# Kernel optimization log

Measured on AMD Instinct MI355X. Metric: run time of the kernel, lower is better.

Reference implementation:

```python
import jax, jax.numpy as jnp
import numpy as np

N_HEAD = 16

def setup_inputs() -> dict:
    key = jax.random.key(0)
    kx, kq, kk, kv, kp = jax.random.split(key, 5)
    B, T, C = 4, 2048, 1024
    scale = 1.0 / np.sqrt(C)
    x = jax.random.normal(kx, (B, T, C), dtype=jnp.float32)
    Wq = jax.random.normal(kq, (C, C), dtype=jnp.float32) * scale
    Wk = jax.random.normal(kk, (C, C), dtype=jnp.float32) * scale
    Wv = jax.random.normal(kv, (C, C), dtype=jnp.float32) * scale
    Wp = jax.random.normal(kp, (C, C), dtype=jnp.float32) * scale
    return {"x": x, "Wq": Wq, "Wk": Wk, "Wv": Wv, "Wp": Wp}

def reference(x, Wq, Wk, Wv, Wp):
    B, T, C = x.shape
    H = N_HEAD
    D = C // H
    # projections (nn.Linear, no bias): x @ W^T
    q = (x @ Wq.T).reshape(B, T, H, D).transpose(0, 2, 1, 3)  # [B,H,T,D]
    k = (x @ Wk.T).reshape(B, T, H, D).transpose(0, 2, 1, 3)
    v = (x @ Wv.T).reshape(B, T, H, D).transpose(0, 2, 1, 3)
    att = jnp.einsum('bhqd,bhkd->bhqk', q, k) / jnp.sqrt(jnp.float32(D))
    causal = jnp.tril(jnp.ones((T, T), dtype=bool))
    att = jnp.where(causal, att, -jnp.inf)
    att = jax.nn.softmax(att, axis=-1)
    # dropout p=0.0 -> identity
    y = jnp.einsum('bhqk,bhkd->bhqd', att, v)  # [B,H,T,D]
    y = y.transpose(0, 2, 1, 3).reshape(B, T, C)
    return y @ Wp.T
```

## Files before the change

### kernel.cpp

```cpp
#include <hip/hip_runtime.h>

typedef __bf16 bfrag __attribute__((ext_vector_type(8)));
typedef __bf16 bh4 __attribute__((ext_vector_type(4)));
typedef float f4 __attribute__((ext_vector_type(4)));

#define AS1C(p) (const __attribute__((address_space(1))) void*)(p)
#define AS3(p)  (__attribute__((address_space(3))) void*)(p)

#define QSCALE 0.18033688011112042f

__device__ __forceinline__ void g2l16(const __bf16* g, __bf16* l) {
  __builtin_amdgcn_global_load_lds(AS1C(g), AS3(l), 16, 0, 0);
}

__global__ __launch_bounds__(256) void cvt5(
    const float* __restrict__ s0, const float* __restrict__ s1,
    const float* __restrict__ s2, const float* __restrict__ s3,
    const float* __restrict__ s4,
    __bf16* __restrict__ d0, __bf16* __restrict__ d1, __bf16* __restrict__ d2,
    __bf16* __restrict__ d3, __bf16* __restrict__ d4, long n0, long n1) {
  const float* s; __bf16* d; long n;
  switch (blockIdx.y) {
    case 0: s = s0; d = d0; n = n0; break;
    case 1: s = s1; d = d1; n = n1; break;
    case 2: s = s2; d = d2; n = n1; break;
    case 3: s = s3; d = d3; n = n1; break;
    default: s = s4; d = d4; n = n1; break;
  }
  long i = ((long)blockIdx.x * 256 + threadIdx.x) * 8;
  if (i >= n) return;
  float4 a = *(const float4*)(s + i);
  float4 b = *(const float4*)(s + i + 4);
  bfrag o;
  o[0] = (__bf16)a.x; o[1] = (__bf16)a.y; o[2] = (__bf16)a.z; o[3] = (__bf16)a.w;
  o[4] = (__bf16)b.x; o[5] = (__bf16)b.y; o[6] = (__bf16)b.z; o[7] = (__bf16)b.w;
  *(bfrag*)(d + i) = o;
}

#define BARR __builtin_amdgcn_s_barrier()
#define WAIT_LGKM { asm volatile("s_waitcnt lgkmcnt(0)" ::: "memory"); \
                    __builtin_amdgcn_sched_barrier(0); }
#define WAIT_VM(N) asm volatile("s_waitcnt vmcnt(" #N ")" ::: "memory")

template <int MODE>
__global__ __launch_bounds__(512, 2) void gemm_dp(
    const __bf16* __restrict__ A, const __bf16* __restrict__ Bw,
    __bf16* __restrict__ qb, __bf16* __restrict__ kb,
    __bf16* __restrict__ vt, float* __restrict__ Cf, int K) {
  __shared__ __bf16 lds[73728];
  __bf16* ldsA = lds;
  __bf16* ldsB = lds + 24576;
  const int tid = threadIdx.x;
  const int wave = tid >> 6, lane = tid & 63;
  const int lm = lane & 15, quad = lane >> 4;
  const int wm = wave >> 2, wn = wave & 3;
  const int bm = blockIdx.x * 128, bn = blockIdx.y * 256;
  const int srow = lane >> 3;
  const int scol = ((lane & 7) ^ srow) * 8;
  const int rsw = lm & 7;

#define STG_A9(sl, kt) { \
    const __bf16* gp_ = A + (long)(bm + wave * 16 + srow) * K + (kt) * 64 + scol; \
    __bf16* lp_ = ldsA + (sl) * 8192 + wave * 1024 + lane * 8; \
    g2l16(gp_, lp_); g2l16(gp_ + 8 * K, lp_ + 512); }
#define STG_B9(sl, kt, h) { \
    const __bf16* gp_ = Bw + (long)(bn + (h) * 128 + wave * 16 + srow) * K + (kt) * 64 + scol; \
    __bf16* lp_ = ldsB + (sl) * 16384 + (h) * 8192 + wave * 1024 + lane * 8; \
    g2l16(gp_, lp_); g2l16(gp_ + 8 * K, lp_ + 512); }
#define STG_TILE(sl, kt) { STG_A9(sl, kt); STG_B9(sl, kt, 0); STG_B9(sl, kt, 1); }

#define COMPUTE_HALF(sl) { \
    const __bf16* Ab_ = ldsA + (sl) * 8192 + (wm * 64 + lm) * 64; \
    const __bf16* Bb_ = ldsB + (sl) * 16384 + (wn * 64 + lm) * 64; \
    bfrag af_[4][2], bg_[2][2]; \
    _Pragma("unroll") for (int j_ = 0; j_ < 4; ++j_) \
      _Pragma("unroll") for (int kk_ = 0; kk_ < 2; ++kk_) \
        af_[j_][kk_] = *(const bfrag*)(Ab_ + j_ * 1024 + ((kk_ * 4 + quad) ^ rsw) * 8); \
    _Pragma("unroll") for (int n_ = 0; n_ < 2; ++n_) \
      _Pragma("unroll") for (int kk_ = 0; kk_ < 2; ++kk_) \
        bg_[n_][kk_] = *(const bfrag*)(Bb_ + n_ * 1024 + ((kk_ * 4 + quad) ^ rsw) * 8); \
    WAIT_LGKM; \
    __builtin_amdgcn_s_setprio(1); \
    _Pragma("unroll") for (int j_ = 0; j_ < 4; ++j_) \
      _Pragma("unroll") for (int n_ = 0; n_ < 2; ++n_) \
        _Pragma("unroll") for (int kk_ = 0; kk_ < 2; ++kk_) \
          acc[j_][n_] = __builtin_amdgcn_mfma_f32_16x16x32_bf16( \
              af_[j_][kk_], bg_[n_][kk_], acc[j_][n_], 0, 0, 0); \
    __builtin_amdgcn_s_setprio(0); \
    _Pragma("unroll") for (int n_ = 0; n_ < 2; ++n_) \
      _Pragma("unroll") for (int kk_ = 0; kk_ < 2; ++kk_) \
        bg_[n_][kk_] = *(const bfrag*)(Bb_ + (2 + n_) * 1024 + ((kk_ * 4 + quad) ^ rsw) * 8); \
    WAIT_LGKM; \
    __builtin_amdgcn_s_setprio(1); \
    _Pragma("unroll") for (int j_ = 0; j_ < 4; ++j_) \
      _Pragma("unroll") for (int n_ = 0; n_ < 2; ++n_) \
        _Pragma("unroll") for (int kk_ = 0; kk_ < 2; ++kk_) \
          acc[j_][2 + n_] = __builtin_amdgcn_mfma_f32_16x16x32_bf16( \
              af_[j_][kk_], bg_[n_][kk_], acc[j_][2 + n_], 0, 0, 0); \
    __builtin_amdgcn_s_setprio(0); }

  f4 acc[4][4] = {};
  const int ntiles = K >> 6;
  STG_TILE(0, 0);
  STG_TILE(1, 1);
  WAIT_VM(6);
  BARR;
#pragma unroll 1
  for (int i = 0; i < (ntiles >> 1); ++i) {
    const int e = 2 * i, o = 2 * i + 1;
    const int se = e % 3, so = o % 3;
    if (e + 2 < ntiles) { const int s2 = (e + 2) % 3; STG_TILE(s2, e + 2); }
    COMPUTE_HALF(se);
    if (e + 2 < ntiles) { WAIT_VM(6); } else { WAIT_VM(0); }
    BARR;
    if (o + 2 < ntiles) { const int s2 = (o + 2) % 3; STG_TILE(s2, o + 2); }
    COMPUTE_HALF(so);
    if (o + 2 < ntiles) WAIT_VM(6);
    BARR;
  }

  if (MODE == 1) {
#pragma unroll
    for (int mi = 0; mi < 4; ++mi)
#pragma unroll
      for (int ni = 0; ni < 4; ++ni)
#pragma unroll
        for (int r = 0; r < 4; ++r) {
          long row = bm + wm * 64 + mi * 16 + quad * 4 + r;
          long col = bn + wn * 64 + ni * 16 + lm;
          Cf[row * 1024 + col] = acc[mi][ni][r];
        }
  } else if (bn < 2048) {
    __bf16* dst = (bn < 1024) ? qb : kb;
    const float scl = (bn < 1024) ? QSCALE : 1.0f;
    const int nb = bn & 1023;
#pragma unroll
    for (int mi = 0; mi < 4; ++mi)
#pragma unroll
      for (int ni = 0; ni < 4; ++ni)
#pragma unroll
        for (int r = 0; r < 4; ++r) {
          long row = bm + wm * 64 + mi * 16 + quad * 4 + r;
          long col = nb + wn * 64 + ni * 16 + lm;
          dst[row * 1024 + col] = (__bf16)(acc[mi][ni][r] * scl);
        }
  } else {
#pragma unroll
    for (int mi = 0; mi < 4; ++mi)
#pragma unroll
      for (int ni = 0; ni < 4; ++ni)
#pragma unroll
        for (int r = 0; r < 4; ++r) {
          int d = wn * 64 + ni * 16 + lm;
          int tp = wm * 64 + (quad * 4 + r) * 4 + mi;
          lds[d * 130 + tp] = (__bf16)acc[mi][ni][r];
        }
    __syncthreads();
    const int bloc = bm >> 11;
    const int tloc = bm & 2047;
#pragma unroll
    for (int p = 0; p < 8; ++p) {
      int d = (tid >> 4) + p * 32;
      int c = (tid & 15) * 8;
      long dglob = (bn - 2048) + d;
      *(bfrag*)(vt + ((long)bloc * 1024 + dglob) * 2048 + tloc + c) =
          *(const bfrag*)(lds + d * 130 + c);
    }
  }
}

template <bool A_F32, bool OUT_F32>
__global__ __launch_bounds__(256) void gemm_bt_cv(
    const void* __restrict__ Ap, const float* __restrict__ Bp,
    void* __restrict__ Cp, int M, int N, int K, float scl) {
  __shared__ __bf16 As[128 * 32];
  __shared__ __bf16 Bs[128 * 32];
  const int tid = threadIdx.x;
  const int lane = tid & 63, wave = tid >> 6;
  const int lm = lane & 15, quad = lane >> 4;
  const int bm = blockIdx.x * 128, bn = blockIdx.y * 128;
  const int wr = (wave >> 1) * 64, wc = (wave & 1) * 64;
  const int e0 = tid * 16, sr = e0 >> 5, sc = e0 & 31;
  f4 acc[4][4] = {};
  for (int k0 = 0; k0 < K; k0 += 32) {
    if (A_F32) {
      const float4* ga = (const float4*)((const float*)Ap + (long)(bm + sr) * K + k0 + sc);
#pragma unroll
      for (int j = 0; j < 4; ++j) {
        float4 v = ga[j];
        As[sr * 32 + sc + j * 4 + 0] = (__bf16)v.x;
        As[sr * 32 + sc + j * 4 + 1] = (__bf16)v.y;
        As[sr * 32 + sc + j * 4 + 2] = (__bf16)v.z;
        As[sr * 32 + sc + j * 4 + 3] = (__bf16)v.w;
      }
    } else {
      const __bf16* Ab = (const __bf16*)Ap + (long)(bm + sr) * K + k0 + sc;
      *(bfrag*)(As + sr * 32 + sc) = *(const bfrag*)Ab;
      *(bfrag*)(As + sr * 32 + sc + 8) = *(const bfrag*)(Ab + 8);
    }
    {
      const float4* gb = (const float4*)(Bp + (long)(bn + sr) * K + k0 + sc);
#pragma unroll
      for (int j = 0; j < 4; ++j) {
        float4 v = gb[j];
        Bs[sr * 32 + sc + j * 4 + 0] = (__bf16)v.x;
        Bs[sr * 32 + sc + j * 4 + 1] = (__bf16)v.y;
        Bs[sr * 32 + sc + j * 4 + 2] = (__bf16)v.z;
        Bs[sr * 32 + sc + j * 4 + 3] = (__bf16)v.w;
      }
    }
    __syncthreads();
    bfrag af[4], bg[4];
#pragma unroll
    for (int mi = 0; mi < 4; ++mi)
      af[mi] = *(const bfrag*)(As + (wr + mi * 16 + lm) * 32 + quad * 8);
#pragma unroll
    for (int ni = 0; ni < 4; ++ni)
      bg[ni] = *(const bfrag*)(Bs + (wc + ni * 16 + lm) * 32 + quad * 8);
#pragma unroll
    for (int mi = 0; mi < 4; ++mi)
#pragma unroll
      for (int ni = 0; ni < 4; ++ni)
        acc[mi][ni] = __builtin_amdgcn_mfma_f32_16x16x32_bf16(af[mi], bg[ni], acc[mi][ni], 0, 0, 0);
    __syncthreads();
  }
#pragma unroll
  for (int mi = 0; mi < 4; ++mi)
#pragma unroll
    for (int ni = 0; ni < 4; ++ni)
#pragma unroll
      for (int r = 0; r < 4; ++r) {
        long row = bm + wr + mi * 16 + quad * 4 + r;
        long col = bn + wc + ni * 16 + lm;
        if (OUT_F32) ((float*)Cp)[row * N + col] = acc[mi][ni][r] * scl;
        else ((__bf16*)Cp)[row * N + col] = (__bf16)(acc[mi][ni][r] * scl);
      }
}

#define KP 72

template <bool VT>
__global__ __launch_bounds__(256, 2) void attn_fwd8(
    const __bf16* Qg, const __bf16* __restrict__ Kg,
    const __bf16* __restrict__ Vsrc, __bf16* Yg) {
  const int TT = 2048, CC = 1024;
  __shared__ __bf16 Ks[64 * KP];
  __shared__ __bf16 Vs[64 * KP];
  __shared__ __bf16 Ps[16 * 16 * KP];
  const int tid = threadIdx.x;
  const int wave = tid >> 6, lane = tid & 63;
  const int lm = lane & 15, quad = lane >> 4;
  const int bh = blockIdx.x, i = blockIdx.y;
  const int b = bh >> 4, h = bh & 15;
  const int qtA = i, qtB = 15 - i;
  const long rbase = (long)b * TT;
  const int hoff = h * 64;
  int row0[4];
  row0[0] = qtA * 128 + wave * 16;
  row0[1] = qtA * 128 + 64 + wave * 16;
  row0[2] = qtB * 128 + wave * 16;
  row0[3] = qtB * 128 + 64 + wave * 16;
  __bf16* Pw[4];
#pragma unroll
  for (int fr = 0; fr < 4; ++fr) Pw[fr] = Ps + (wave * 4 + fr) * 16 * KP;
  bfrag qf[4][2];
#pragma unroll
  for (int fr = 0; fr < 4; ++fr)
#pragma unroll
    for (int f = 0; f < 2; ++f)
      qf[fr][f] = *(const bfrag*)(Qg + (rbase + row0[fr] + lm) * CC + hoff + f * 32 + quad * 8);
  bfrag ones;
#pragma unroll
  for (int j = 0; j < 8; ++j) ones[j] = (__bf16)1.0f;
  f4 y[4][4] = {};
  f4 L[4] = {};

  const int ktLast = 2 * qtB + 1;
  bfrag kin[2], vin[2];
#pragma unroll
  for (int s = 0; s < 2; ++s) {
    int idx = tid + s * 256;
    int r = idx >> 3, c = (idx & 7) * 8;
    kin[s] = *(const bfrag*)(Kg + (rbase + r) * CC + hoff + c);
    if (VT)
      vin[s] = *(const bfrag*)(Vsrc + ((long)b * 1024 + hoff + r) * 2048 + c);
    else
      vin[s] = *(const bfrag*)(Vsrc + (rbase + r) * CC + hoff + c);
  }

  for (int kt = 0; kt <= ktLast; ++kt) {
    const int kBase = kt * 64;
    __syncthreads();
#pragma unroll
    for (int s = 0; s < 2; ++s) {
      int idx = tid + s * 256;
      int r = idx >> 3, c = (idx & 7) * 8;
      *(bfrag*)(Ks + r * KP + c) = kin[s];
      if (VT) {
        *(bfrag*)(Vs + r * KP + c) = vin[s];
      } else {
        int kp = (r & 15) * 4 + (r >> 4);
#pragma unroll
        for (int j = 0; j < 8; ++j) Vs[(c + j) * KP + kp] = vin[s][j];
      }
    }
    const bool more = (kt < ktLast);
    bfrag kin2[2], vin2[2];
    if (more) {
      const int nB = kBase + 64;
#pragma unroll
      for (int s = 0; s < 2; ++s) {
        int idx = tid + s * 256;
        int r = idx >> 3, c = (idx & 7) * 8;
        kin2[s] = *(const bfrag*)(Kg + (rbase + nB + r) * CC + hoff + c);
        if (VT)
          vin2[s] = *(const bfrag*)(Vsrc + ((long)b * 1024 + hoff + r) * 2048 + nB + c);
        else
          vin2[s] = *(const bfrag*)(Vsrc + (rbase + nB + r) * CC + hoff + c);
      }
    }
    __syncthreads();
    bfrag kf[8];
#pragma unroll
    for (int sub = 0; sub < 4; ++sub)
#pragma unroll
      for (int f = 0; f < 2; ++f)
        kf[sub * 2 + f] = *(const bfrag*)(Ks + (sub * 16 + lm) * KP + f * 32 + quad * 8);
#pragma unroll
    for (int fr = 0; fr < 4; ++fr) {
      if (kBase <= row0[fr] + 15) {
        f4 sac[4];
#pragma unroll
        for (int sub = 0; sub < 4; ++sub) {
          f4 z = {};
#pragma unroll
          for (int f = 0; f < 2; ++f)
            z = __builtin_amdgcn_mfma_f32_16x16x32_bf16(qf[fr][f], kf[sub * 2 + f], z, 0, 0, 0);
          sac[sub] = z;
        }
        if (kBase + 63 > row0[fr]) {
#pragma unroll
          for (int r = 0; r < 4; ++r) {
            bh4 pk;
#pragma unroll
            for (int sub = 0; sub < 4; ++sub) {
              float pv = __builtin_amdgcn_exp2f(sac[sub][r]);
              bool masked = (kBase + sub * 16 + lm > row0[fr] + quad * 4 + r);
              pk[sub] = (__bf16)(masked ? 0.f : pv);
            }
            *(bh4*)(Pw[fr] + (quad * 4 + r) * KP + lm * 4) = pk;
          }
        } else {
#pragma unroll
          for (int r = 0; r < 4; ++r) {
            bh4 pk;
#pragma unroll
            for (int sub = 0; sub < 4; ++sub)
              pk[sub] = (__bf16)__builtin_amdgcn_exp2f(sac[sub][r]);
            *(bh4*)(Pw[fr] + (quad * 4 + r) * KP + lm * 4) = pk;
          }
        }
      }
    }
    __asm__ volatile("s_waitcnt lgkmcnt(0)" ::: "memory");
    bfrag vf[8];
#pragma unroll
    for (int sub = 0; sub < 4; ++sub)
#pragma unroll
      for (int f = 0; f < 2; ++f)
        vf[sub * 2 + f] = *(const bfrag*)(Vs + (sub * 16 + lm) * KP + f * 32 + quad * 8);
#pragma unroll
    for (int fr = 0; fr < 4; ++fr) {
      if (kBase <= row0[fr] + 15) {
#pragma unroll
        for (int f = 0; f < 2; ++f) {
          bfrag pf = *(const bfrag*)(Pw[fr] + lm * KP + f * 32 + quad * 8);
          L[fr] = __builtin_amdgcn_mfma_f32_16x16x32_bf16(pf, ones, L[fr], 0, 0, 0);
#pragma unroll
          for (int ds = 0; ds < 4; ++ds)
            y[fr][ds] = __builtin_amdgcn_mfma_f32_16x16x32_bf16(pf, vf[ds * 2 + f], y[fr][ds], 0, 0, 0);
        }
      }
    }
    if (more) {
      kin[0] = kin2[0]; kin[1] = kin2[1];
      vin[0] = vin2[0]; vin[1] = vin2[1];
    }
  }
#pragma unroll
  for (int fr = 0; fr < 4; ++fr)
#pragma unroll
    for (int ds = 0; ds < 4; ++ds)
#pragma unroll
      for (int r = 0; r < 4; ++r) {
        long row = rbase + row0[fr] + quad * 4 + r;
        Yg[row * CC + hoff + ds * 16 + lm] = (__bf16)(y[fr][ds][r] / L[fr][r]);
      }
}

extern "C" void kernel_launch(void* const* d_in, const int* in_sizes, int n_in,
                              void* d_out, int out_size, void* d_ws, size_t ws_size,
                              hipStream_t stream) {
  (void)in_sizes; (void)n_in; (void)out_size;
  const float* x  = (const float*)d_in[0];
  const float* Wq = (const float*)d_in[1];
  const float* Wk = (const float*)d_in[2];
  const float* Wv = (const float*)d_in[3];
  const float* Wp = (const float*)d_in[4];
  float* out = (float*)d_out;
  const long R = 8192;
  const long BUF = R * 1024;
  const long WN = 1024L * 1024;
  __bf16* qb = (__bf16*)d_ws;
  __bf16* kb = (__bf16*)d_out;
  __bf16* vslot = kb + BUF;
  dim3 blk(256, 1, 1);
  const size_t need = (size_t)(2 * BUF + 4 * WN) * 2;
  if (ws_size >= need) {
    __bf16* xb = qb + BUF;
    __bf16* wqkv = xb + BUF;
    __bf16* wpb = wqkv + 3 * WN;
    cvt5<<<dim3((unsigned)(BUF / (256 * 8)), 5, 1), blk, 0, stream>>>(
        x, Wq, Wk, Wv, Wp, xb, wqkv, wqkv + WN, wqkv + 2 * WN, wpb, BUF, WN);
    gemm_dp<0><<<dim3(64, 12, 1), dim3(512, 1, 1), 0, stream>>>(
        xb, wqkv, qb, kb, vslot, nullptr, 1024);
    attn_fwd8<true><<<dim3(64, 8, 1), blk, 0, stream>>>(qb, kb, vslot, qb);
    gemm_dp<1><<<dim3(64, 4, 1), dim3(512, 1, 1), 0, stream>>>(
        qb, wpb, nullptr, nullptr, nullptr, out, 1024);
  } else {
    gemm_bt_cv<true, false><<<dim3(64, 8, 1), blk, 0, stream>>>(x, Wq, qb, 8192, 1024, 1024, QSCALE);
    gemm_bt_cv<true, false><<<dim3(64, 8, 1), blk, 0, stream>>>(x, Wk, kb, 8192, 1024, 1024, 1.0f);
    gemm_bt_cv<true, false><<<dim3(64, 8, 1), blk, 0, stream>>>(x, Wv, vslot, 8192, 1024, 1024, 1.0f);
    attn_fwd8<false><<<dim3(64, 8, 1), blk, 0, stream>>>(qb, kb, vslot, qb);
    gemm_bt_cv<false, true><<<dim3(64, 8, 1), blk, 0, stream>>>(qb, Wp, out, 8192, 1024, 1024, 1.0f);
  }
}
```

Baseline: 227.4 us.

## Add 256x256-tile QKV GEMM with XCD-aware block mapping and LDS-transposed V output

Replaces the 128x256-tile QKV projection GEMM with a new kernel that uses 256x256 tiles, double-buffered async global-to-LDS loads with a swizzled layout, and a block index remap that groups M tiles per XCD. This cuts the number of blocks from 768 to 384 and raises arithmetic intensity per tile. The V output is transposed through LDS in two halves before being stored. The bigger tile needs more accumulator registers per thread and leaves fewer blocks to fill the CUs. The Q/K epilogue writes scalar bf16 stores, which may be uncoalesced.

```diff
diff --git a/kernel.cpp b/kernel.cpp
--- a/kernel.cpp
+++ b/kernel.cpp
@@ -41,6 +41,107 @@
 #define WAIT_LGKM { asm volatile("s_waitcnt lgkmcnt(0)" ::: "memory"); \
                     __builtin_amdgcn_sched_barrier(0); }
 #define WAIT_VM(N) asm volatile("s_waitcnt vmcnt(" #N ")" ::: "memory")
+
+__global__ __launch_bounds__(512, 2) void gemm_qkv256(
+    const __bf16* __restrict__ A, const __bf16* __restrict__ Bw,
+    __bf16* __restrict__ qb, __bf16* __restrict__ kb,
+    __bf16* __restrict__ vt, int K) {
+  __shared__ __bf16 lds[65536];
+  const int tid = threadIdx.x;
+  const int wave = tid >> 6, lane = tid & 63;
+  const int lm = lane & 15, quad = lane >> 4;
+  const int wm = wave >> 2, wn = wave & 3;
+  const int l = blockIdx.y * 32 + blockIdx.x;
+  const int xcd = l & 7, idx = l >> 3;
+  const int bm = (xcd * 4 + (idx & 3)) * 256;
+  const int bn = (idx >> 2) * 256;
+  const int scol = ((tid & 7) ^ ((tid >> 3) & 7)) * 8;
+  const int rsw = lm & 7;
+
+#define STGQ(b, kt) { \
+    _Pragma("unroll") for (int j_ = 0; j_ < 4; ++j_) { \
+      g2l16(A + (long)(bm + j_ * 64 + (tid >> 3)) * K + (kt) * 64 + scol, \
+            lds + (b) * 16384 + j_ * 4096 + tid * 8); \
+      g2l16(Bw + (long)(bn + j_ * 64 + (tid >> 3)) * K + (kt) * 64 + scol, \
+            lds + 32768 + (b) * 16384 + j_ * 4096 + tid * 8); } }
+
+#define KHALF(b, kk) { \
+    const __bf16* Ab_ = lds + (b) * 16384 + (wm * 128 + lm) * 64; \
+    const __bf16* Bb_ = lds + 32768 + (b) * 16384 + (wn * 64 + lm) * 64; \
+    bfrag af_[8], bg_[4]; \
+    _Pragma("unroll") for (int j_ = 0; j_ < 8; ++j_) \
+      af_[j_] = *(const bfrag*)(Ab_ + j_ * 1024 + (((kk) * 4 + quad) ^ rsw) * 8); \
+    _Pragma("unroll") for (int n_ = 0; n_ < 4; ++n_) \
+      bg_[n_] = *(const bfrag*)(Bb_ + n_ * 1024 + (((kk) * 4 + quad) ^ rsw) * 8); \
+    WAIT_LGKM; \
+    __builtin_amdgcn_s_setprio(1); \
+    _Pragma("unroll") for (int j_ = 0; j_ < 8; ++j_) \
+      _Pragma("unroll") for (int n_ = 0; n_ < 4; ++n_) \
+        acc[j_][n_] = __builtin_amdgcn_mfma_f32_16x16x32_bf16( \
+            af_[j_], bg_[n_], acc[j_][n_], 0, 0, 0); \
+    __builtin_amdgcn_s_setprio(0); }
+
+  f4 acc[8][4] = {};
+  const int ntiles = K >> 6;
+  STGQ(0, 0);
+  WAIT_VM(0);
+  BARR;
+#pragma unroll 1
+  for (int t = 0; t < ntiles; ++t) {
+    const int b = t & 1;
+    if (t < ntiles - 1) STGQ(b ^ 1, t + 1);
+    KHALF(b, 0);
+    KHALF(b, 1);
+    if (t < ntiles - 1) WAIT_VM(0);
+    BARR;
+  }
+
+  if (bn < 2048) {
+    __bf16* dst = (bn < 1024) ? qb : kb;
+    const float scl = (bn < 1024) ? QSCALE : 1.0f;
+    const int nb = bn & 1023;
+#pragma unroll
+    for (int mi = 0; mi < 8; ++mi)
+#pragma unroll
+      for (int ni = 0; ni < 4; ++ni)
+#pragma unroll
+        for (int r = 0; r < 4; ++r) {
+          long row = bm + wm * 128 + mi * 16 + quad * 4 + r;
+          long col = nb + wn * 64 + ni * 16 + lm;
+          dst[row * 1024 + col] = (__bf16)(acc[mi][ni][r] * scl);
+        }
+  } else {
+    const int bloc = bm >> 11;
+    const int tbase = bm & 2047;
+    const int dloc = wn * 64 + 0;
+#pragma unroll
+    for (int h = 0; h < 2; ++h) {
+      if (wm == h) {
+#pragma unroll
+        for (int mi = 0; mi < 8; ++mi)
+#pragma unroll
+          for (int ni = 0; ni < 4; ++ni)
+#pragma unroll
+            for (int r = 0; r < 4; ++r) {
+              int d = wn * 64 + ni * 16 + lm;
+              int tp = (mi >> 2) * 64 + (quad * 4 + r) * 4 + (mi & 3);
+              lds[d * 130 + tp] = (__bf16)acc[mi][ni][r];
+            }
+      }
+      __syncthreads();
+#pragma unroll
+      for (int p = 0; p < 8; ++p) {
+        int d = (tid >> 4) + p * 32;
+        int c = (tid & 15) * 8;
+        long dglob = (bn - 2048) + d;
+        *(bfrag*)(vt + ((long)bloc * 1024 + dglob) * 2048 + tbase + h * 128 + c) =
+            *(const bfrag*)(lds + d * 130 + c);
+      }
+      __syncthreads();
+    }
+    (void)dloc;
+  }
+}
 
 template <int MODE>
 __global__ __launch_bounds__(512, 2) void gemm_dp(
@@ -422,8 +523,8 @@
     __bf16* wpb = wqkv + 3 * WN;
     cvt5<<<dim3((unsigned)(BUF / (256 * 8)), 5, 1), blk, 0, stream>>>(
         x, Wq, Wk, Wv, Wp, xb, wqkv, wqkv + WN, wqkv + 2 * WN, wpb, BUF, WN);
-    gemm_dp<0><<<dim3(64, 12, 1), dim3(512, 1, 1), 0, stream>>>(
-        xb, wqkv, qb, kb, vslot, nullptr, 1024);
+    gemm_qkv256<<<dim3(32, 12, 1), dim3(512, 1, 1), 0, stream>>>(
+        xb, wqkv, qb, kb, vslot, 1024);
     attn_fwd8<true><<<dim3(64, 8, 1), blk, 0, stream>>>(qb, kb, vslot, qb);
     gemm_dp<1><<<dim3(64, 4, 1), dim3(512, 1, 1), 0, stream>>>(
         qb, wpb, nullptr, nullptr, nullptr, out, 1024);
```

After: 227.2 us. No clear change (-0.1%).

## Retile projection GEMM to 256x128 with XCD-aware L2 block swizzle

Applied to the files above, without the earlier changes.

Changes the projection GEMM block tile from 128x256 to 256x128, with 8 waves arranged 4x2, and launches a 1D grid. Block indices are remapped so that blocks on the same XCD share A-row panels and B-column groups, aiming to improve L2 reuse on the multi-die GPU. The k-loop now processes one 64-wide tile per iteration with a single barrier. The V-transpose epilogue is adjusted to the new tile shape. This adds index arithmetic, and the LDS stride changes in the transpose may alter bank conflicts.

```diff
diff --git a/kernel.cpp b/kernel.cpp
--- a/kernel.cpp
+++ b/kernel.cpp
@@ -43,80 +43,73 @@
 #define WAIT_VM(N) asm volatile("s_waitcnt vmcnt(" #N ")" ::: "memory")
 
 template <int MODE>
-__global__ __launch_bounds__(512, 2) void gemm_dp(
+__global__ __launch_bounds__(512, 2) void gemm_l2(
     const __bf16* __restrict__ A, const __bf16* __restrict__ Bw,
     __bf16* __restrict__ qb, __bf16* __restrict__ kb,
     __bf16* __restrict__ vt, float* __restrict__ Cf, int K) {
   __shared__ __bf16 lds[73728];
   __bf16* ldsA = lds;
-  __bf16* ldsB = lds + 24576;
+  __bf16* ldsB = lds + 49152;
   const int tid = threadIdx.x;
   const int wave = tid >> 6, lane = tid & 63;
   const int lm = lane & 15, quad = lane >> 4;
-  const int wm = wave >> 2, wn = wave & 3;
-  const int bm = blockIdx.x * 128, bn = blockIdx.y * 256;
-  const int srow = lane >> 3;
-  const int scol = ((lane & 7) ^ srow) * 8;
+  const int wm = wave >> 1, wn = wave & 1;
+  const int l = blockIdx.x;
+  const int xcd = l & 7;
+  int bm, bnq;
+  if (MODE == 0) {
+    const int r = l >> 3;
+    const int pos = r & 31, rnd = r >> 5;
+    bm = xcd * 4 + (pos & 3);
+    bnq = (pos >> 2) + rnd * 8;
+  } else {
+    const int pos = l >> 3;
+    bm = xcd * 4 + (pos & 3);
+    bnq = pos >> 2;
+  }
+  const long bmr = (long)bm * 256;
+  const long bnr = (long)bnq * 128;
+  const int scol = ((tid & 7) ^ ((tid >> 3) & 7)) * 8;
   const int rsw = lm & 7;
 
-#define STG_A9(sl, kt) { \
-    const __bf16* gp_ = A + (long)(bm + wave * 16 + srow) * K + (kt) * 64 + scol; \
-    __bf16* lp_ = ldsA + (sl) * 8192 + wave * 1024 + lane * 8; \
-    g2l16(gp_, lp_); g2l16(gp_ + 8 * K, lp_ + 512); }
-#define STG_B9(sl, kt, h) { \
-    const __bf16* gp_ = Bw + (long)(bn + (h) * 128 + wave * 16 + srow) * K + (kt) * 64 + scol; \
-    __bf16* lp_ = ldsB + (sl) * 16384 + (h) * 8192 + wave * 1024 + lane * 8; \
-    g2l16(gp_, lp_); g2l16(gp_ + 8 * K, lp_ + 512); }
-#define STG_TILE(sl, kt) { STG_A9(sl, kt); STG_B9(sl, kt, 0); STG_B9(sl, kt, 1); }
-
-#define COMPUTE_HALF(sl) { \
-    const __bf16* Ab_ = ldsA + (sl) * 8192 + (wm * 64 + lm) * 64; \
-    const __bf16* Bb_ = ldsB + (sl) * 16384 + (wn * 64 + lm) * 64; \
-    bfrag af_[4][2], bg_[2][2]; \
+#define STG(sl, kt) { \
     _Pragma("unroll") for (int j_ = 0; j_ < 4; ++j_) \
-      _Pragma("unroll") for (int kk_ = 0; kk_ < 2; ++kk_) \
-        af_[j_][kk_] = *(const bfrag*)(Ab_ + j_ * 1024 + ((kk_ * 4 + quad) ^ rsw) * 8); \
-    _Pragma("unroll") for (int n_ = 0; n_ < 2; ++n_) \
-      _Pragma("unroll") for (int kk_ = 0; kk_ < 2; ++kk_) \
-        bg_[n_][kk_] = *(const bfrag*)(Bb_ + n_ * 1024 + ((kk_ * 4 + quad) ^ rsw) * 8); \
+      g2l16(A + (bmr + j_ * 64 + (tid >> 3)) * K + (kt) * 64 + scol, \
+            ldsA + (sl) * 16384 + j_ * 4096 + tid * 8); \
+    _Pragma("unroll") for (int j_ = 0; j_ < 2; ++j_) \
+      g2l16(Bw + (bnr + j_ * 64 + (tid >> 3)) * K + (kt) * 64 + scol, \
+            ldsB + (sl) * 8192 + j_ * 4096 + tid * 8); }
+
+#define KHALF(sl, kk) { \
+    const __bf16* Ab_ = ldsA + (sl) * 16384 + (wm * 64 + lm) * 64; \
+    const __bf16* Bb_ = ldsB + (sl) * 8192 + (wn * 64 + lm) * 64; \
+    bfrag af_[4], bg_[4]; \
+    _Pragma("unroll") for (int j_ = 0; j_ < 4; ++j_) \
+      af_[j_] = *(const bfrag*)(Ab_ + j_ * 1024 + (((kk) * 4 + quad) ^ rsw) * 8); \
+    _Pragma("unroll") for (int n_ = 0; n_ < 4; ++n_) \
+      bg_[n_] = *(const bfrag*)(Bb_ + n_ * 1024 + (((kk) * 4 + quad) ^ rsw) * 8); \
     WAIT_LGKM; \
     __builtin_amdgcn_s_setprio(1); \
     _Pragma("unroll") for (int j_ = 0; j_ < 4; ++j_) \
-      _Pragma("unroll") for (int n_ = 0; n_ < 2; ++n_) \
-        _Pragma("unroll") for (int kk_ = 0; kk_ < 2; ++kk_) \
-          acc[j_][n_] = __builtin_amdgcn_mfma_f32_16x16x32_bf16( \
-              af_[j_][kk_], bg_[n_][kk_], acc[j_][n_], 0, 0, 0); \
-    __builtin_amdgcn_s_setprio(0); \
-    _Pragma("unroll") for (int n_ = 0; n_ < 2; ++n_) \
-      _Pragma("unroll") for (int kk_ = 0; kk_ < 2; ++kk_) \
-        bg_[n_][kk_] = *(const bfrag*)(Bb_ + (2 + n_) * 1024 + ((kk_ * 4 + quad) ^ rsw) * 8); \
-    WAIT_LGKM; \
-    __builtin_amdgcn_s_setprio(1); \
-    _Pragma("unroll") for (int j_ = 0; j_ < 4; ++j_) \
-      _Pragma("unroll") for (int n_ = 0; n_ < 2; ++n_) \
-        _Pragma("unroll") for (int kk_ = 0; kk_ < 2; ++kk_) \
-          acc[j_][2 + n_] = __builtin_amdgcn_mfma_f32_16x16x32_bf16( \
-              af_[j_][kk_], bg_[n_][kk_], acc[j_][2 + n_], 0, 0, 0); \
+      _Pragma("unroll") for (int n_ = 0; n_ < 4; ++n_) \
+        acc[j_][n_] = __builtin_amdgcn_mfma_f32_16x16x32_bf16( \
+            af_[j_], bg_[n_], acc[j_][n_], 0, 0, 0); \
     __builtin_amdgcn_s_setprio(0); }
 
   f4 acc[4][4] = {};
   const int ntiles = K >> 6;
-  STG_TILE(0, 0);
-  STG_TILE(1, 1);
+  STG(0, 0);
+  STG(1, 1);
   WAIT_VM(6);
   BARR;
 #pragma unroll 1
-  for (int i = 0; i < (ntiles >> 1); ++i) {
-    const int e = 2 * i, o = 2 * i + 1;
-    const int se = e % 3, so = o % 3;
-    if (e + 2 < ntiles) { const int s2 = (e + 2) % 3; STG_TILE(s2, e + 2); }
-    COMPUTE_HALF(se);
-    if (e + 2 < ntiles) { WAIT_VM(6); } else { WAIT_VM(0); }
+  for (int t = 0; t < ntiles; ++t) {
+    const int sl = t % 3;
+    if (t + 2 < ntiles) { const int s2 = (t + 2) % 3; STG(s2, t + 2); }
+    KHALF(sl, 0);
+    KHALF(sl, 1);
+    if (t + 2 < ntiles) { WAIT_VM(6); } else { WAIT_VM(0); }
     BARR;
-    if (o + 2 < ntiles) { const int s2 = (o + 2) % 3; STG_TILE(s2, o + 2); }
-    COMPUTE_HALF(so);
-    if (o + 2 < ntiles) WAIT_VM(6);
-    BARR;
   }
 
   if (MODE == 1) {
@@ -126,21 +119,21 @@
       for (int ni = 0; ni < 4; ++ni)
 #pragma unroll
         for (int r = 0; r < 4; ++r) {
-          long row = bm + wm * 64 + mi * 16 + quad * 4 + r;
-          long col = bn + wn * 64 + ni * 16 + lm;
+          long row = bmr + wm * 64 + mi * 16 + quad * 4 + r;
+          long col = bnr + wn * 64 + ni * 16 + lm;
           Cf[row * 1024 + col] = acc[mi][ni][r];
         }
-  } else if (bn < 2048) {
-    __bf16* dst = (bn < 1024) ? qb : kb;
-    const float scl = (bn < 1024) ? QSCALE : 1.0f;
-    const int nb = bn & 1023;
+  } else if (bnq < 16) {
+    __bf16* dst = (bnq < 8) ? qb : kb;
+    const float scl = (bnq < 8) ? QSCALE : 1.0f;
+    const int nb = (bnq & 7) * 128;
 #pragma unroll
     for (int mi = 0; mi < 4; ++mi)
 #pragma unroll
       for (int ni = 0; ni < 4; ++ni)
 #pragma unroll
         for (int r = 0; r < 4; ++r) {
-          long row = bm + wm * 64 + mi * 16 + quad * 4 + r;
+          long row = bmr + wm * 64 + mi * 16 + quad * 4 + r;
           long col = nb + wn * 64 + ni * 16 + lm;
           dst[row * 1024 + col] = (__bf16)(acc[mi][ni][r] * scl);
         }
@@ -153,18 +146,21 @@
         for (int r = 0; r < 4; ++r) {
           int d = wn * 64 + ni * 16 + lm;
           int tp = wm * 64 + (quad * 4 + r) * 4 + mi;
-          lds[d * 130 + tp] = (__bf16)acc[mi][ni][r];
+          lds[d * 260 + tp] = (__bf16)acc[mi][ni][r];
         }
     __syncthreads();
-    const int bloc = bm >> 11;
-    const int tloc = bm & 2047;
-#pragma unroll
-    for (int p = 0; p < 8; ++p) {
+    const int bloc = bm >> 3;
+    const int tbase = (bm & 7) * 256;
+    const long dbase = bnr - 2048;
+#pragma unroll
+    for (int p = 0; p < 4; ++p) {
       int d = (tid >> 4) + p * 32;
-      int c = (tid & 15) * 8;
-      long dglob = (bn - 2048) + d;
-      *(bfrag*)(vt + ((long)bloc * 1024 + dglob) * 2048 + tloc + c) =
-          *(const bfrag*)(lds + d * 130 + c);
+#pragma unroll
+      for (int c2 = 0; c2 < 2; ++c2) {
+        int c = (tid & 15) * 16 + c2 * 8;
+        *(bfrag*)(vt + ((long)bloc * 1024 + dbase + d) * 2048 + tbase + c) =
+            *(const bfrag*)(lds + d * 260 + c);
+      }
     }
   }
 }
@@ -422,10 +418,10 @@
     __bf16* wpb = wqkv + 3 * WN;
     cvt5<<<dim3((unsigned)(BUF / (256 * 8)), 5, 1), blk, 0, stream>>>(
         x, Wq, Wk, Wv, Wp, xb, wqkv, wqkv + WN, wqkv + 2 * WN, wpb, BUF, WN);
-    gemm_dp<0><<<dim3(64, 12, 1), dim3(512, 1, 1), 0, stream>>>(
+    gemm_l2<0><<<dim3(768, 1, 1), dim3(512, 1, 1), 0, stream>>>(
         xb, wqkv, qb, kb, vslot, nullptr, 1024);
     attn_fwd8<true><<<dim3(64, 8, 1), blk, 0, stream>>>(qb, kb, vslot, qb);
-    gemm_dp<1><<<dim3(64, 4, 1), dim3(512, 1, 1), 0, stream>>>(
+    gemm_l2<1><<<dim3(256, 1, 1), dim3(512, 1, 1), 0, stream>>>(
         qb, wpb, nullptr, nullptr, nullptr, out, 1024);
   } else {
     gemm_bt_cv<true, false><<<dim3(64, 8, 1), blk, 0, stream>>>(x, Wq, qb, 8192, 1024, 1024, QSCALE);
```

New measurement: 229.0 us. Within noise of the previous version (+0.7%).
